# Kernel tuning notes

Measured on AMD Instinct MI355X. Metric: run time of the kernel, lower is better.

## Reference

```python
import jax, jax.numpy as jnp
import numpy as np

MAX_LEN = 1024
DIM = 1024
NUM_HEADS = 16
DIM_HEAD = 64
BATCH = 8


def _pos_emb(max_len, dim):
    pos_seq = jnp.arange(max_len - 1, -1, -1.0, dtype=jnp.float32)
    inv_freq = 1.0 / (10000.0 ** (jnp.arange(0, dim, 2.0, dtype=jnp.float32) / dim))
    sinusoid = jnp.einsum('i,j->ij', pos_seq, inv_freq)
    return jnp.concatenate([jnp.sin(sinusoid), jnp.cos(sinusoid)], axis=-1)  # [S, dim]


def _rel_shift(x):
    # x: [B, H, I, J] -> Transformer-XL relative shift
    b, h, i, j = x.shape
    x = jnp.pad(x, ((0, 0), (0, 0), (0, 0), (1, 0)))
    x = x.reshape(b, h, j + 1, i)[:, :, 1:, :]
    return x.reshape(b, h, i, j)


def setup_inputs() -> dict:
    key = jax.random.key(0)
    k1, k2, k3, k4 = jax.random.split(key, 4)
    inputs = jax.random.normal(k1, (BATCH, MAX_LEN, DIM), dtype=jnp.float32)
    mask = jnp.ones((BATCH, MAX_LEN), dtype=bool)
    Wqkv = jax.random.normal(k2, (DIM, 3 * NUM_HEADS * DIM_HEAD), dtype=jnp.float32) * 0.02
    Wr = jax.random.normal(k3, (DIM, NUM_HEADS * DIM_HEAD), dtype=jnp.float32) * 0.02
    Wo = jax.random.normal(k4, (NUM_HEADS * DIM_HEAD, DIM), dtype=jnp.float32) * 0.02
    return {"inputs": inputs, "mask": mask, "Wqkv": Wqkv, "Wr": Wr, "Wo": Wo}


def reference(inputs, mask, Wqkv, Wr, Wo):
    B, S, dim = inputs.shape
    H, Dh = NUM_HEADS, DIM_HEAD
    scale = 1.0 / (Dh ** 0.5)

    qkv = jnp.einsum('bsd,de->bse', inputs, Wqkv)  # [B,S,3*H*Dh]
    q, k, v = jnp.split(qkv, 3, axis=-1)
    q = q.reshape(B, S, H, Dh)
    k = k.reshape(B, S, H, Dh)
    v = v.reshape(B, S, H, Dh)

    pos = _pos_emb(S, dim)                          # [S, dim]
    r = jnp.einsum('sd,de->se', pos, Wr).reshape(S, H, Dh)  # [S,H,Dh]

    AC = jnp.einsum('bihd,bjhd->bhij', q, k)        # content score
    BD = jnp.einsum('bihd,jhd->bhij', q, r)         # position score
    BD = _rel_shift(BD)
    score = (AC + BD) * scale

    att_mask = mask[:, None, None, :].astype(score.dtype)
    score = score * att_mask - 1e30 * (1.0 - att_mask)

    prob = jax.nn.softmax(score, axis=-1)
    attn_vec = jnp.einsum('bhij,bjhd->bihd', prob, v).reshape(B, S, H * Dh)
    out = jnp.einsum('bse,ed->bsd', attn_vec, Wo)
    return out + inputs
```

## Files before the change

### kernel.cpp

```cpp
#include <hip/hip_runtime.h>

#define SQL 1024
#define NHD 16
#define DHD 64
#define NB  8

typedef unsigned char u8;
typedef unsigned short u16;
typedef short s16x8 __attribute__((ext_vector_type(8)));
typedef __bf16 b16x8 __attribute__((ext_vector_type(8)));
typedef float f32x4 __attribute__((ext_vector_type(4)));
typedef u16 u16x4 __attribute__((ext_vector_type(4)));
typedef u16 u16x8 __attribute__((ext_vector_type(8)));
typedef unsigned int u32x4 __attribute__((ext_vector_type(4)));

static __device__ __forceinline__ u16 f2b(float f) {
  __bf16 h = (__bf16)f;
  return __builtin_bit_cast(u16, h);
}
static __device__ __forceinline__ float b2f(u16 v) {
  return __uint_as_float(((unsigned)v) << 16);
}

#if __has_builtin(__builtin_amdgcn_cvt_pk_fp8_f32)
static __device__ __forceinline__ u8 f2fp8(float f) {
  return (u8)(__builtin_amdgcn_cvt_pk_fp8_f32(f, f, 0, false) & 0xff);
}
#else
static __device__ __forceinline__ u8 f2fp8(float f) {
  f = fminf(fmaxf(f, -448.f), 448.f);
  unsigned s = (__float_as_uint(f) >> 31) << 7;
  float a = fabsf(f);
  if (a < 0.0009765625f) return (u8)s;
  int e; float m = frexpf(a, &e);
  if (e - 1 < -6) {
    int q = (int)(a * 512.f + 0.5f);
    return (u8)(s | q);
  }
  int q = (int)(m * 16.f + 0.5f);
  if (q == 16) { q = 8; ++e; }
  int ef = e - 1 + 7;
  if (ef > 15) { ef = 15; q = 14; }
  return (u8)(s | (ef << 3) | (q - 8));
}
#endif

#if __has_builtin(__builtin_amdgcn_cvt_f32_fp8)
static __device__ __forceinline__ f32x4 fp8dec4(unsigned w) {
  f32x4 r;
  r[0] = __builtin_amdgcn_cvt_f32_fp8(w, 0);
  r[1] = __builtin_amdgcn_cvt_f32_fp8(w, 1);
  r[2] = __builtin_amdgcn_cvt_f32_fp8(w, 2);
  r[3] = __builtin_amdgcn_cvt_f32_fp8(w, 3);
  return r;
}
#else
static __device__ __forceinline__ float fp8dec1(unsigned b) {
  unsigned s = (b >> 7) & 1, e = (b >> 3) & 15, m = b & 7;
  float v = (e == 0) ? (float)m * 0.001953125f
                     : (float)(8 + m) * exp2f((float)((int)e - 10));
  return s ? -v : v;
}
static __device__ __forceinline__ f32x4 fp8dec4(unsigned w) {
  f32x4 r;
  r[0] = fp8dec1(w & 0xff);
  r[1] = fp8dec1((w >> 8) & 0xff);
  r[2] = fp8dec1((w >> 16) & 0xff);
  r[3] = fp8dec1((w >> 24) & 0xff);
  return r;
}
#endif

template <typename V>
static __device__ __forceinline__ auto mfma_sel(V a, V b, f32x4 c, int)
    -> decltype(__builtin_amdgcn_mfma_f32_16x16x32_bf16(a, b, c, 0, 0, 0)) {
  return __builtin_amdgcn_mfma_f32_16x16x32_bf16(a, b, c, 0, 0, 0);
}
template <typename V>
static __device__ __forceinline__ f32x4 mfma_sel(V a, V b, f32x4 c, long) {
  return __builtin_amdgcn_mfma_f32_16x16x32_bf16(
      __builtin_bit_cast(b16x8, a), __builtin_bit_cast(b16x8, b), c, 0, 0, 0);
}
static __device__ __forceinline__ f32x4 MFMA(s16x8 a, s16x8 b, f32x4 c) {
  return mfma_sel(a, b, c, 0);
}

static __device__ __forceinline__ void gload16(const u16* g, u16* l) {
  __builtin_amdgcn_global_load_lds(
      (const __attribute__((address_space(1))) unsigned int*)g,
      (__attribute__((address_space(3))) unsigned int*)l, 16, 0, 0);
}

__global__ __launch_bounds__(256) void cvt_kernel(const float* __restrict__ src,
                                                  u16* __restrict__ dst, int n4) {
  int idx = blockIdx.x * 256 + threadIdx.x;
  if (idx < n4) {
    f32x4 v = reinterpret_cast<const f32x4*>(src)[idx];
    u16x4 o;
    o[0] = f2b(v[0]); o[1] = f2b(v[1]); o[2] = f2b(v[2]); o[3] = f2b(v[3]);
    reinterpret_cast<u16x4*>(dst)[idx] = o;
  }
}

__global__ __launch_bounds__(256) void transpose_cvt(const float* __restrict__ src,
                                                     u16* __restrict__ dst,
                                                     int R, int C) {
  __shared__ float tile[32][33];
  int bx = blockIdx.x * 32;
  int by = blockIdx.y * 32;
  int tx = threadIdx.x & 31, ty = threadIdx.x >> 5;
  #pragma unroll
  for (int r = ty; r < 32; r += 8)
    tile[r][tx] = src[(size_t)(by + r) * C + bx + tx];
  __syncthreads();
  #pragma unroll
  for (int r = ty; r < 32; r += 8)
    dst[(size_t)(bx + r) * R + by + tx] = f2b(tile[tx][r]);
}

__global__ __launch_bounds__(256) void pos_kernel(u16* __restrict__ posb) {
  int idx = blockIdx.x * 256 + threadIdx.x;
  int s = idx >> 10, j = idx & 1023;
  int t = (j < 512) ? j : j - 512;
  float freq = __expf(-(float)(2 * t) * (logf(10000.f) / 1024.f));
  float ang = (float)(1023 - s) * freq;
  posb[idx] = f2b((j < 512) ? sinf(ang) : cosf(ang));
}

__global__ __launch_bounds__(256) void vt_kernel(const u16* __restrict__ qkv,
                                                 u16* __restrict__ vT) {
  int bh = blockIdx.x;
  int b = bh >> 4, h = bh & 15;
  int j0 = blockIdx.y * 64;
  __shared__ __align__(16) u16 tile[64][72];
  int tid = threadIdx.x;
  for (int idx = tid; idx < 512; idx += 256) {
    int j = idx >> 3, c = (idx & 7) * 8;
    *reinterpret_cast<u32x4*>(&tile[j][c]) = *reinterpret_cast<const u32x4*>(
        &qkv[(size_t)(b * SQL + j0 + j) * 3072 + 2048 + h * 64 + c]);
  }
  __syncthreads();
  for (int idx = tid; idx < 512; idx += 256) {
    int d = idx >> 3, c = (idx & 7) * 8;
    u16x8 pk;
    #pragma unroll
    for (int e = 0; e < 8; ++e) pk[e] = tile[c + e][d];
    *reinterpret_cast<u16x8*>(
        &vT[(size_t)bh * DHD * SQL + (size_t)d * SQL + j0 + c]) = pk;
  }
}

template <int OUT>
__global__ __launch_bounds__(256) void gemm97(
    const u16* __restrict__ A, const u16* __restrict__ Bt, void* __restrict__ Cv,
    const float* __restrict__ resid, int K, int lda, int ldb, int ldc,
    int bandH) {
  __shared__ __align__(16) u16 at[128 * 64];
  __shared__ __align__(16) u16 bt[128 * 64];

  int bid = blockIdx.x;
  int xcd = bid & 7, loc = bid >> 3;
  int m0 = (xcd * bandH + (loc % bandH)) * 128;
  int n0 = (loc / bandH) * 128;

  const int tid = threadIdx.x, lane = tid & 63, w = tid >> 6;
  const int wm = (w & 1) * 64, wn = (w >> 1) * 64;
  const int fr = lane & 15, kg = lane >> 4;
  const int lrow = lane >> 3, lcol = (lane & 7) * 8;

  f32x4 acc[4][4] = {};

  for (int k0 = 0; k0 < K; k0 += 64) {
    __syncthreads();
    #pragma unroll
    for (int ci = 0; ci < 4; ++ci) {
      int ch = w * 4 + ci;
      gload16(&A[(size_t)(m0 + ch * 8 + lrow) * lda + k0 + lcol], &at[ch * 512]);
      gload16(&Bt[(size_t)(n0 + ch * 8 + lrow) * ldb + k0 + lcol], &bt[ch * 512]);
    }
    __syncthreads();

    #pragma unroll
    for (int ks = 0; ks < 2; ++ks) {
      s16x8 af[4], bf[4];
      #pragma unroll
      for (int i = 0; i < 4; ++i) {
        af[i] = *(const s16x8*)&at[(wm + i * 16 + fr) * 64 + ks * 32 + kg * 8];
        bf[i] = *(const s16x8*)&bt[(wn + i * 16 + fr) * 64 + ks * 32 + kg * 8];
      }
      #pragma unroll
      for (int mi = 0; mi < 4; ++mi)
        #pragma unroll
        for (int ni = 0; ni < 4; ++ni)
          acc[mi][ni] = MFMA(af[mi], bf[ni], acc[mi][ni]);
    }
  }

  #pragma unroll
  for (int mi = 0; mi < 4; ++mi)
    #pragma unroll
    for (int ni = 0; ni < 4; ++ni)
      #pragma unroll
      for (int rr = 0; rr < 4; ++rr) {
        int rrow = m0 + wm + mi * 16 + kg * 4 + rr;
        int ccol = n0 + wn + ni * 16 + fr;
        size_t ci = (size_t)rrow * ldc + ccol;
        float v = acc[mi][ni][rr];
        if constexpr (OUT == 1) ((u16*)Cv)[ci] = f2b(v);
        else ((float*)Cv)[ci] = v + resid[ci];
      }
}

#define TLD 72
#define SC2 0.180336880f
#define THRU 64.0f

__global__ __launch_bounds__(256, 4) void fused_attn_bd(
    const u16* __restrict__ qkv, const u16* __restrict__ rb,
    u8* __restrict__ cbbd, const u8* __restrict__ cbat,
    const u16* __restrict__ vT, u16* __restrict__ att,
    int zbd, int zat, int nat, int CH) {
  __shared__ __align__(16) u16 smem[13824];
  const int bid = blockIdx.x;
  const int tid = threadIdx.x, lane = tid & 63, w = tid >> 6;
  const int fr = lane & 15, kg = lane >> 4;

  if (bid >= nat) {
    u16* at = smem;
    u16* bt = smem + 5120;
    int loc = bid - nat;
    int zloc = loc >> 6;
    int m0 = (loc & 7) * 128;
    int n0 = ((loc >> 3) & 7) * 128;
    int zg = zbd + zloc;
    int bb = zg >> 4, hh = zg & 15;
    const u16* A = qkv + (size_t)bb * SQL * 3072 + (size_t)hh * 64;
    const u16* Bt = rb + (size_t)hh * 64;
    u8* bd = cbbd + (size_t)zloc * SQL * SQL;

    const int wm = (w >> 1) * 64;
    const int wn = (w & 1) * 64;
    const int kb = kg * 8;

    f32x4 acc[4][4] = {};
    for (int k0 = 0; k0 < 64; k0 += 32) {
      __syncthreads();
      for (int idx = tid; idx < 512; idx += 256) {
        int r = idx >> 2, c = (idx & 3) << 3;
        *(u32x4*)&at[r * 40 + c] =
            *(const u32x4*)&A[(size_t)(m0 + r) * 3072 + k0 + c];
        *(u32x4*)&bt[r * 40 + c] =
            *(const u32x4*)&Bt[(size_t)(n0 + r) * 1024 + k0 + c];
      }
      __syncthreads();

      s16x8 af[4], bfr[4];
      #pragma unroll
      for (int mi = 0; mi < 4; ++mi)
        af[mi] = *(const s16x8*)&at[(wm + mi * 16 + fr) * 40 + kb];
      #pragma unroll
      for (int ni = 0; ni < 4; ++ni)
        bfr[ni] = *(const s16x8*)&bt[(wn + ni * 16 + fr) * 40 + kb];
      #pragma unroll
      for (int mi = 0; mi < 4; ++mi)
        #pragma unroll
        for (int ni = 0; ni < 4; ++ni)
          acc[mi][ni] = MFMA(af[mi], bfr[ni], acc[mi][ni]);
    }

    const int orow = kg << 2;
    const int ocol = fr;
    #pragma unroll
    for (int mi = 0; mi < 4; ++mi)
      #pragma unroll
      for (int ni = 0; ni < 4; ++ni)
        #pragma unroll
        for (int rr = 0; rr < 4; ++rr) {
          int rrow = m0 + wm + mi * 16 + orow + rr;
          int ccol = n0 + wn + ni * 16 + ocol;
          u8 bv = f2fp8(acc[mi][ni][rr]);
          int j1 = rrow + ccol - (SQL - 1);
          if (j1 >= 0) bd[(size_t)rrow * SQL + j1] = bv;
          int j2 = rrow + ccol + 1;
          if (rrow >= 1 && j2 < SQL) bd[(size_t)(rrow - 1) * SQL + j2] = bv;
        }
    if (n0 == 0 && tid < 128) {
      int i = m0 + tid;
      if (i + 1 < SQL) bd[(size_t)i * SQL + i + 1] = 0;
    }
    return;
  }

  u16* kl = smem;
  u16* vl = smem + 4608;
  u16* pl = smem + 9216;

  int per = CH * 2;
  int swz = (bid & 7) * per + (bid >> 3);
  int z = swz >> 4, qt = swz & 15;
  int bh = zat + z;
  int b = bh >> 4, h = bh & 15;
  int i0 = qt * 64;

  const int kb8 = kg * 8;
  const int srow = tid >> 3, sc8 = (tid & 7) * 8;
  const int myrow = w * 16 + fr;

  s16x8 aq[2];
  {
    const u16* qp = &qkv[(size_t)(b * SQL + i0 + myrow) * 3072 + h * 64 + kb8];
    aq[0] = *(const s16x8*)qp;
    aq[1] = *(const s16x8*)(qp + 32);
  }

  const u16* kbase = &qkv[(size_t)(b * SQL) * 3072 + 1024 + h * 64];
  const u16* vbase = &vT[(size_t)bh * 64 * 1024];
  const u8* bdrow = &cbat[(size_t)z * SQL * SQL + (size_t)(i0 + myrow) * SQL + kg * 4];

  u32x4 kA0, kA1, vA0, vA1;
  u32x4 kB0, kB1, vB0, vB1;
  unsigned dA0, dA1, dA2, dA3;
  unsigned dB0, dB1, dB2, dB3;

  auto ISSUE_KV = [&](u32x4& K0, u32x4& K1, u32x4& V0, u32x4& V1, int t) {
    int j0 = t * 64;
    K0 = *(const u32x4*)&kbase[(size_t)(j0 + srow) * 3072 + sc8];
    K1 = *(const u32x4*)&kbase[(size_t)(j0 + srow + 32) * 3072 + sc8];
    V0 = *(const u32x4*)&vbase[(size_t)srow * 1024 + j0 + sc8];
    V1 = *(const u32x4*)&vbase[(size_t)(srow + 32) * 1024 + j0 + sc8];
  };
  auto ISSUE_BD = [&](unsigned& D0, unsigned& D1, unsigned& D2, unsigned& D3,
                      int t) {
    const u8* p = bdrow + t * 64;
    D0 = *(const unsigned*)(p);
    D1 = *(const unsigned*)(p + 16);
    D2 = *(const unsigned*)(p + 32);
    D3 = *(const unsigned*)(p + 48);
  };
  auto COMMIT = [&](u32x4 K0, u32x4 K1, u32x4 V0, u32x4 V1) {
    *(u32x4*)&kl[srow * TLD + sc8] = K0;
    *(u32x4*)&kl[(srow + 32) * TLD + sc8] = K1;
    *(u32x4*)&vl[srow * TLD + sc8] = V0;
    *(u32x4*)&vl[(srow + 32) * TLD + sc8] = V1;
  };

  f32x4 acco[4] = {};
  float mreg = -1e30f, lreg = 0.f;

  auto BODY = [&](int j0, unsigned d0, unsigned d1, unsigned d2, unsigned d3) {
    f32x4 st[4] = {};
    #pragma unroll
    for (int nf = 0; nf < 4; ++nf)
      #pragma unroll
      for (int ks = 0; ks < 2; ++ks)
        st[nf] = MFMA(*(const s16x8*)&kl[(nf * 16 + fr) * TLD + ks * 32 + kb8],
                      aq[ks], st[nf]);

    f32x4 bdv[4] = {fp8dec4(d0), fp8dec4(d1), fp8dec4(d2), fp8dec4(d3)};
    float s0[4][4];
    float rmax = -1e30f;
    #pragma unroll
    for (int nf = 0; nf < 4; ++nf) {
      #pragma unroll
      for (int rr = 0; rr < 4; ++rr) {
        s0[nf][rr] = st[nf][rr] + bdv[nf][rr];
        rmax = fmaxf(rmax, s0[nf][rr]);
      }
    }
    rmax = fmaxf(rmax, __shfl_xor(rmax, 16));
    rmax = fmaxf(rmax, __shfl_xor(rmax, 32));
    if (rmax > mreg + THRU) {
      float sf = exp2f((mreg - rmax) * SC2);
      mreg = rmax;
      lreg *= sf;
      #pragma unroll
      for (int mf = 0; mf < 4; ++mf) acco[mf] *= sf;
    }
    const float C = -mreg * SC2;
    float ps = 0.f;
    #pragma unroll
    for (int nf = 0; nf < 4; ++nf) {
      u16x4 pp;
      #pragma unroll
      for (int rr = 0; rr < 4; ++rr) {
        float p = exp2f(__builtin_fmaf(s0[nf][rr], SC2, C));
        ps += p;
        pp[rr] = f2b(p);
      }
      *(u16x4*)&pl[myrow * TLD + nf * 16 + kg * 4] = pp;
    }
    ps += __shfl_xor(ps, 16);
    ps += __shfl_xor(ps, 32);
    lreg += ps;

    s16x8 ap0 = *(const s16x8*)&pl[myrow * TLD + kb8];
    s16x8 ap1 = *(const s16x8*)&pl[myrow * TLD + 32 + kb8];
    #pragma unroll
    for (int mf = 0; mf < 4; ++mf) {
      acco[mf] = MFMA(*(const s16x8*)&vl[(mf * 16 + fr) * TLD + kb8], ap0,
                      acco[mf]);
      acco[mf] = MFMA(*(const s16x8*)&vl[(mf * 16 + fr) * TLD + 32 + kb8], ap1,
                      acco[mf]);
    }
  };

  ISSUE_KV(kA0, kA1, vA0, vA1, 0);
  ISSUE_BD(dA0, dA1, dA2, dA3, 0);
  for (int tt = 0; tt < 16; tt += 2) {
    __syncthreads();
    COMMIT(kA0, kA1, vA0, vA1);
    __syncthreads();
    ISSUE_KV(kB0, kB1, vB0, vB1, tt + 1);
    ISSUE_BD(dB0, dB1, dB2, dB3, tt + 1);
    BODY(tt * 64, dA0, dA1, dA2, dA3);

    __syncthreads();
    COMMIT(kB0, kB1, vB0, vB1);
    __syncthreads();
    if (tt < 14) {
      ISSUE_KV(kA0, kA1, vA0, vA1, tt + 2);
      ISSUE_BD(dA0, dA1, dA2, dA3, tt + 2);
    }
    BODY((tt + 1) * 64, dB0, dB1, dB2, dB3);
  }

  {
    float inv = 1.0f / lreg;
    size_t base = (size_t)(b * SQL + i0 + myrow) * 1024 + h * 64;
    #pragma unroll
    for (int mf = 0; mf < 4; ++mf) {
      u16x4 o;
      #pragma unroll
      for (int rr = 0; rr < 4; ++rr) o[rr] = f2b(acco[mf][rr] * inv);
      *(u16x4*)&att[base + mf * 16 + kg * 4] = o;
    }
  }
}

extern "C" void kernel_launch(void* const* d_in, const int* in_sizes, int n_in,
                              void* d_out, int out_size, void* d_ws, size_t ws_size,
                              hipStream_t stream) {
  const float* inputs = (const float*)d_in[0];
  const float* Wqkv = (const float*)d_in[2];
  const float* Wr = (const float*)d_in[3];
  const float* Wo = (const float*)d_in[4];
  float* out = (float*)d_out;

  char* ws = (char*)d_ws;
  size_t off = 0;
  auto alloc = [&](size_t bytes) -> char* {
    char* p = ws + off;
    off = (off + bytes + 255) & ~(size_t)255;
    return p;
  };
  u16* qkvb = (u16*)alloc(8192ULL * 3072 * 2);
  u16* vT   = (u16*)alloc(128ULL * 64 * 1024 * 2);
  u16* att  = (u16*)alloc(8192ULL * 1024 * 2);
  u16* rb   = (u16*)alloc(1024ULL * 1024 * 2);
  u16* WoT  = (u16*)alloc(1024ULL * 1024 * 2);

  size_t remain = (ws_size > off) ? (ws_size - off) : 0;
  char* tbase = ws + off;
  u16* Xb    = (u16*)tbase;
  u16* WqkvT = (u16*)(tbase + 16777216);
  u16* WrT   = (u16*)(tbase + 16777216 + 6291456);
  u16* posb  = (u16*)(tbase + 16777216 + 6291456 + 2097152);

  int CH = 8;
  const int cands[4] = {64, 32, 16, 8};
  for (int t = 0; t < 4; ++t) {
    if ((size_t)cands[t] * SQL * SQL * 2 + 1024 <= remain) { CH = cands[t]; break; }
  }
  u8* cbufA = (u8*)tbase;
  u8* cbufB = cbufA + (size_t)CH * SQL * SQL;

  cvt_kernel<<<dim3(8192), dim3(256), 0, stream>>>(inputs, Xb, 8192 * 1024 / 4);
  transpose_cvt<<<dim3(96, 32), dim3(256), 0, stream>>>(Wqkv, WqkvT, 1024, 3072);
  transpose_cvt<<<dim3(32, 32), dim3(256), 0, stream>>>(Wr, WrT, 1024, 1024);
  transpose_cvt<<<dim3(32, 32), dim3(256), 0, stream>>>(Wo, WoT, 1024, 1024);
  pos_kernel<<<dim3(4096), dim3(256), 0, stream>>>(posb);

  gemm97<1><<<dim3(64), dim3(256), 0, stream>>>(
      posb, WrT, rb, nullptr, 1024, 1024, 1024, 1024, 1);
  gemm97<1><<<dim3(1536), dim3(256), 0, stream>>>(
      Xb, WqkvT, qkvb, nullptr, 1024, 1024, 1024, 3072, 8);
  vt_kernel<<<dim3(128, 16), dim3(256), 0, stream>>>(qkvb, vT);

  int nch = 128 / CH;
  for (int r = 0; r <= nch; ++r) {
    int nbd = (r < nch) ? 64 * CH : 0;
    int nat = (r >= 1) ? CH * 16 : 0;
    u8* cbbd = (r & 1) ? cbufB : cbufA;
    u8* cbat = (r & 1) ? cbufA : cbufB;
    fused_attn_bd<<<dim3(nat + nbd), dim3(256), 0, stream>>>(
        qkvb, rb, cbbd, cbat, vT, att, r * CH, (r - 1) * CH, nat, CH);
  }

  gemm97<2><<<dim3(512), dim3(256), 0, stream>>>(
      att, WoT, out, inputs, 1024, 1024, 1024, 1024, 8);
}
```

Before: 341.5 us.

## Store raw BD rows in flat skewed buffer and apply rel-shift at read time

The BD producer blocks now compute Q·R^T per 64-row query tile, streaming R tiles through LDS. They write contiguous rows of packed fp8 (four values per store) into a flat buffer with a 1028-byte row stride, replacing the scattered per-byte writes that applied the relative shift. The attention consumer recovers the shifted values by reading two unaligned word pairs and funnel-shifting them, with a per-element fallback on the diagonal tile. This is meant to cut write traffic and scattered-store cost in the producer. It adds shift and alignment logic and extra loads in the consumer's inner loop.

```diff
diff --git a/kernel.cpp b/kernel.cpp
--- a/kernel.cpp
+++ b/kernel.cpp
@@ -4,9 +4,11 @@
 #define NHD 16
 #define DHD 64
 #define NB  8
+#define HB  1053700ULL
 
 typedef unsigned char u8;
 typedef unsigned short u16;
+typedef unsigned long long u64;
 typedef short s16x8 __attribute__((ext_vector_type(8)));
 typedef __bf16 b16x8 __attribute__((ext_vector_type(8)));
 typedef float f32x4 __attribute__((ext_vector_type(4)));
@@ -23,8 +25,9 @@
 }
 
 #if __has_builtin(__builtin_amdgcn_cvt_pk_fp8_f32)
-static __device__ __forceinline__ u8 f2fp8(float f) {
-  return (u8)(__builtin_amdgcn_cvt_pk_fp8_f32(f, f, 0, false) & 0xff);
+static __device__ __forceinline__ unsigned pack4_fp8(f32x4 v) {
+  unsigned t0 = __builtin_amdgcn_cvt_pk_fp8_f32(v[0], v[1], 0, false);
+  return __builtin_amdgcn_cvt_pk_fp8_f32(v[2], v[3], t0, true);
 }
 #else
 static __device__ __forceinline__ u8 f2fp8(float f) {
@@ -33,15 +36,16 @@
   float a = fabsf(f);
   if (a < 0.0009765625f) return (u8)s;
   int e; float m = frexpf(a, &e);
-  if (e - 1 < -6) {
-    int q = (int)(a * 512.f + 0.5f);
-    return (u8)(s | q);
-  }
+  if (e - 1 < -6) { int q = (int)(a * 512.f + 0.5f); return (u8)(s | q); }
   int q = (int)(m * 16.f + 0.5f);
   if (q == 16) { q = 8; ++e; }
   int ef = e - 1 + 7;
   if (ef > 15) { ef = 15; q = 14; }
   return (u8)(s | (ef << 3) | (q - 8));
+}
+static __device__ __forceinline__ unsigned pack4_fp8(f32x4 v) {
+  return (unsigned)f2fp8(v[0]) | ((unsigned)f2fp8(v[1]) << 8) |
+         ((unsigned)f2fp8(v[2]) << 16) | ((unsigned)f2fp8(v[3]) << 24);
 }
 #endif
 
@@ -53,6 +57,9 @@
   r[2] = __builtin_amdgcn_cvt_f32_fp8(w, 2);
   r[3] = __builtin_amdgcn_cvt_f32_fp8(w, 3);
   return r;
+}
+static __device__ __forceinline__ float fp8dec1(unsigned b) {
+  return __builtin_amdgcn_cvt_f32_fp8(b, 0);
 }
 #else
 static __device__ __forceinline__ float fp8dec1(unsigned b) {
@@ -224,69 +231,62 @@
   const int bid = blockIdx.x;
   const int tid = threadIdx.x, lane = tid & 63, w = tid >> 6;
   const int fr = lane & 15, kg = lane >> 4;
+  const int kb8 = kg * 8;
+  const int srow = tid >> 3, sc8 = (tid & 7) * 8;
+  const int myrow = w * 16 + fr;
 
   if (bid >= nat) {
-    u16* at = smem;
-    u16* bt = smem + 5120;
+    u16* rl = smem;
     int loc = bid - nat;
-    int zloc = loc >> 6;
-    int m0 = (loc & 7) * 128;
-    int n0 = ((loc >> 3) & 7) * 128;
-    int zg = zbd + zloc;
-    int bb = zg >> 4, hh = zg & 15;
-    const u16* A = qkv + (size_t)bb * SQL * 3072 + (size_t)hh * 64;
-    const u16* Bt = rb + (size_t)hh * 64;
-    u8* bd = cbbd + (size_t)zloc * SQL * SQL;
-
-    const int wm = (w >> 1) * 64;
-    const int wn = (w & 1) * 64;
-    const int kb = kg * 8;
-
-    f32x4 acc[4][4] = {};
-    for (int k0 = 0; k0 < 64; k0 += 32) {
+    int z = loc >> 4, qt = loc & 15;
+    int bh = zbd + z;
+    int b = bh >> 4, h = bh & 15;
+    int i0 = qt * 64;
+
+    s16x8 aq[2];
+    {
+      const u16* qp = &qkv[(size_t)(b * SQL + i0 + myrow) * 3072 + h * 64 + kb8];
+      aq[0] = *(const s16x8*)qp;
+      aq[1] = *(const s16x8*)(qp + 32);
+    }
+    const u16* rbase = rb + h * 64;
+    u8* frp = cbbd + (size_t)z * HB + (size_t)(i0 + myrow) * 1028;
+
+    u32x4 rA0, rA1, rB0, rB1;
+    auto ISSUE_R = [&](u32x4& R0, u32x4& R1, int t) {
+      R0 = *(const u32x4*)&rbase[(size_t)(t * 64 + srow) * 1024 + sc8];
+      R1 = *(const u32x4*)&rbase[(size_t)(t * 64 + srow + 32) * 1024 + sc8];
+    };
+    auto COMMIT_R = [&](u32x4 R0, u32x4 R1) {
+      *(u32x4*)&rl[srow * TLD + sc8] = R0;
+      *(u32x4*)&rl[(srow + 32) * TLD + sc8] = R1;
+    };
+    auto CBODY = [&](int mt) {
+      f32x4 ct[4] = {};
+      #pragma unroll
+      for (int nf = 0; nf < 4; ++nf)
+        #pragma unroll
+        for (int ks = 0; ks < 2; ++ks)
+          ct[nf] = MFMA(*(const s16x8*)&rl[(nf * 16 + fr) * TLD + ks * 32 + kb8],
+                        aq[ks], ct[nf]);
+      u8* dst = frp + mt * 64 + kg * 4;
+      #pragma unroll
+      for (int nf = 0; nf < 4; ++nf)
+        *(unsigned*)(dst + nf * 16) = pack4_fp8(ct[nf]);
+    };
+
+    ISSUE_R(rA0, rA1, 0);
+    for (int tt = 0; tt < 16; tt += 2) {
       __syncthreads();
-      for (int idx = tid; idx < 512; idx += 256) {
-        int r = idx >> 2, c = (idx & 3) << 3;
-        *(u32x4*)&at[r * 40 + c] =
-            *(const u32x4*)&A[(size_t)(m0 + r) * 3072 + k0 + c];
-        *(u32x4*)&bt[r * 40 + c] =
-            *(const u32x4*)&Bt[(size_t)(n0 + r) * 1024 + k0 + c];
-      }
+      COMMIT_R(rA0, rA1);
       __syncthreads();
-
-      s16x8 af[4], bfr[4];
-      #pragma unroll
-      for (int mi = 0; mi < 4; ++mi)
-        af[mi] = *(const s16x8*)&at[(wm + mi * 16 + fr) * 40 + kb];
-      #pragma unroll
-      for (int ni = 0; ni < 4; ++ni)
-        bfr[ni] = *(const s16x8*)&bt[(wn + ni * 16 + fr) * 40 + kb];
-      #pragma unroll
-      for (int mi = 0; mi < 4; ++mi)
-        #pragma unroll
-        for (int ni = 0; ni < 4; ++ni)
-          acc[mi][ni] = MFMA(af[mi], bfr[ni], acc[mi][ni]);
-    }
-
-    const int orow = kg << 2;
-    const int ocol = fr;
-    #pragma unroll
-    for (int mi = 0; mi < 4; ++mi)
-      #pragma unroll
-      for (int ni = 0; ni < 4; ++ni)
-        #pragma unroll
-        for (int rr = 0; rr < 4; ++rr) {
-          int rrow = m0 + wm + mi * 16 + orow + rr;
-          int ccol = n0 + wn + ni * 16 + ocol;
-          u8 bv = f2fp8(acc[mi][ni][rr]);
-          int j1 = rrow + ccol - (SQL - 1);
-          if (j1 >= 0) bd[(size_t)rrow * SQL + j1] = bv;
-          int j2 = rrow + ccol + 1;
-          if (rrow >= 1 && j2 < SQL) bd[(size_t)(rrow - 1) * SQL + j2] = bv;
-        }
-    if (n0 == 0 && tid < 128) {
-      int i = m0 + tid;
-      if (i + 1 < SQL) bd[(size_t)i * SQL + i + 1] = 0;
+      ISSUE_R(rB0, rB1, tt + 1);
+      CBODY(tt);
+      __syncthreads();
+      COMMIT_R(rB0, rB1);
+      __syncthreads();
+      if (tt < 14) ISSUE_R(rA0, rA1, tt + 2);
+      CBODY(tt + 1);
     }
     return;
   }
@@ -301,26 +301,26 @@
   int bh = zat + z;
   int b = bh >> 4, h = bh & 15;
   int i0 = qt * 64;
-
-  const int kb8 = kg * 8;
-  const int srow = tid >> 3, sc8 = (tid & 7) * 8;
-  const int myrow = w * 16 + fr;
+  const int ig = i0 + myrow;
 
   s16x8 aq[2];
   {
-    const u16* qp = &qkv[(size_t)(b * SQL + i0 + myrow) * 3072 + h * 64 + kb8];
+    const u16* qp = &qkv[(size_t)(b * SQL + ig) * 3072 + h * 64 + kb8];
     aq[0] = *(const s16x8*)qp;
     aq[1] = *(const s16x8*)(qp + 32);
   }
 
   const u16* kbase = &qkv[(size_t)(b * SQL) * 3072 + 1024 + h * 64];
   const u16* vbase = &vT[(size_t)bh * 64 * 1024];
-  const u8* bdrow = &cbat[(size_t)z * SQL * SQL + (size_t)(i0 + myrow) * SQL + kg * 4];
+  const u8* cbz = cbat + (size_t)z * HB;
+  const size_t Bbase = (size_t)ig * 1027 + 1023 + kg * 4;
+  const unsigned sh1 = (unsigned)(Bbase & 3) * 8;
+  const unsigned sh2 = (unsigned)((Bbase + 3) & 3) * 8;
 
   u32x4 kA0, kA1, vA0, vA1;
   u32x4 kB0, kB1, vB0, vB1;
-  unsigned dA0, dA1, dA2, dA3;
-  unsigned dB0, dB1, dB2, dB3;
+  unsigned a0, a1, a2, a3, a4, a5, a6, a7;
+  unsigned c0, c1, c2, c3, c4, c5, c6, c7;
 
   auto ISSUE_KV = [&](u32x4& K0, u32x4& K1, u32x4& V0, u32x4& V1, int t) {
     int j0 = t * 64;
@@ -329,13 +329,15 @@
     V0 = *(const u32x4*)&vbase[(size_t)srow * 1024 + j0 + sc8];
     V1 = *(const u32x4*)&vbase[(size_t)(srow + 32) * 1024 + j0 + sc8];
   };
-  auto ISSUE_BD = [&](unsigned& D0, unsigned& D1, unsigned& D2, unsigned& D3,
+  auto ISSUE_BD = [&](unsigned& W0, unsigned& W1, unsigned& W2, unsigned& W3,
+                      unsigned& W4, unsigned& W5, unsigned& W6, unsigned& W7,
                       int t) {
-    const u8* p = bdrow + t * 64;
-    D0 = *(const unsigned*)(p);
-    D1 = *(const unsigned*)(p + 16);
-    D2 = *(const unsigned*)(p + 32);
-    D3 = *(const unsigned*)(p + 48);
+    size_t A0 = (Bbase + (size_t)(t * 64) + ((t > qt) ? 3 : 0)) & ~(size_t)3;
+    const u8* p = cbz + A0;
+    W0 = *(const unsigned*)(p);      W1 = *(const unsigned*)(p + 4);
+    W2 = *(const unsigned*)(p + 16); W3 = *(const unsigned*)(p + 20);
+    W4 = *(const unsigned*)(p + 32); W5 = *(const unsigned*)(p + 36);
+    W6 = *(const unsigned*)(p + 48); W7 = *(const unsigned*)(p + 52);
   };
   auto COMMIT = [&](u32x4 K0, u32x4 K1, u32x4 V0, u32x4 V1) {
     *(u32x4*)&kl[srow * TLD + sc8] = K0;
@@ -347,7 +349,8 @@
   f32x4 acco[4] = {};
   float mreg = -1e30f, lreg = 0.f;
 
-  auto BODY = [&](int j0, unsigned d0, unsigned d1, unsigned d2, unsigned d3) {
+  auto BODY = [&](int t, unsigned W0, unsigned W1, unsigned W2, unsigned W3,
+                  unsigned W4, unsigned W5, unsigned W6, unsigned W7) {
     f32x4 st[4] = {};
     #pragma unroll
     for (int nf = 0; nf < 4; ++nf)
@@ -356,7 +359,30 @@
         st[nf] = MFMA(*(const s16x8*)&kl[(nf * 16 + fr) * TLD + ks * 32 + kb8],
                       aq[ks], st[nf]);
 
-    f32x4 bdv[4] = {fp8dec4(d0), fp8dec4(d1), fp8dec4(d2), fp8dec4(d3)};
+    f32x4 bdv[4];
+    if (t == qt) {
+      #pragma unroll
+      for (int nf = 0; nf < 4; ++nf)
+        #pragma unroll
+        for (int rr = 0; rr < 4; ++rr) {
+          int joff = nf * 16 + kg * 4 + rr;
+          float v;
+          if (joff == myrow + 1) v = 0.f;
+          else {
+            size_t P = (size_t)ig * 1027 + (size_t)(qt * 64 + joff) +
+                       ((joff <= myrow) ? 1023 : 1026);
+            v = fp8dec1((unsigned)cbz[P]);
+          }
+          bdv[nf][rr] = v;
+        }
+    } else {
+      unsigned sh = (t > qt) ? sh2 : sh1;
+      bdv[0] = fp8dec4((unsigned)((((u64)W1 << 32) | W0) >> sh));
+      bdv[1] = fp8dec4((unsigned)((((u64)W3 << 32) | W2) >> sh));
+      bdv[2] = fp8dec4((unsigned)((((u64)W5 << 32) | W4) >> sh));
+      bdv[3] = fp8dec4((unsigned)((((u64)W7 << 32) | W6) >> sh));
+    }
+
     float s0[4][4];
     float rmax = -1e30f;
     #pragma unroll
@@ -405,28 +431,28 @@
   };
 
   ISSUE_KV(kA0, kA1, vA0, vA1, 0);
-  ISSUE_BD(dA0, dA1, dA2, dA3, 0);
+  ISSUE_BD(a0, a1, a2, a3, a4, a5, a6, a7, 0);
   for (int tt = 0; tt < 16; tt += 2) {
     __syncthreads();
     COMMIT(kA0, kA1, vA0, vA1);
     __syncthreads();
     ISSUE_KV(kB0, kB1, vB0, vB1, tt + 1);
-    ISSUE_BD(dB0, dB1, dB2, dB3, tt + 1);
-    BODY(tt * 64, dA0, dA1, dA2, dA3);
+    ISSUE_BD(c0, c1, c2, c3, c4, c5, c6, c7, tt + 1);
+    BODY(tt, a0, a1, a2, a3, a4, a5, a6, a7);
 
     __syncthreads();
     COMMIT(kB0, kB1, vB0, vB1);
     __syncthreads();
     if (tt < 14) {
       ISSUE_KV(kA0, kA1, vA0, vA1, tt + 2);
-      ISSUE_BD(dA0, dA1, dA2, dA3, tt + 2);
-    }
-    BODY((tt + 1) * 64, dB0, dB1, dB2, dB3);
+      ISSUE_BD(a0, a1, a2, a3, a4, a5, a6, a7, tt + 2);
+    }
+    BODY(tt + 1, c0, c1, c2, c3, c4, c5, c6, c7);
   }
 
   {
     float inv = 1.0f / lreg;
-    size_t base = (size_t)(b * SQL + i0 + myrow) * 1024 + h * 64;
+    size_t base = (size_t)(b * SQL + ig) * 1024 + h * 64;
     #pragma unroll
     for (int mf = 0; mf < 4; ++mf) {
       u16x4 o;
@@ -469,10 +495,10 @@
   int CH = 8;
   const int cands[4] = {64, 32, 16, 8};
   for (int t = 0; t < 4; ++t) {
-    if ((size_t)cands[t] * SQL * SQL * 2 + 1024 <= remain) { CH = cands[t]; break; }
+    if ((size_t)cands[t] * HB * 2 + 1024 <= remain) { CH = cands[t]; break; }
   }
   u8* cbufA = (u8*)tbase;
-  u8* cbufB = cbufA + (size_t)CH * SQL * SQL;
+  u8* cbufB = cbufA + (size_t)CH * HB;
 
   cvt_kernel<<<dim3(8192), dim3(256), 0, stream>>>(inputs, Xb, 8192 * 1024 / 4);
   transpose_cvt<<<dim3(96, 32), dim3(256), 0, stream>>>(Wqkv, WqkvT, 1024, 3072);
@@ -488,7 +514,7 @@
 
   int nch = 128 / CH;
   for (int r = 0; r <= nch; ++r) {
-    int nbd = (r < nch) ? 64 * CH : 0;
+    int nbd = (r < nch) ? CH * 16 : 0;
     int nat = (r >= 1) ? CH * 16 : 0;
     u8* cbbd = (r & 1) ? cbufB : cbufA;
     u8* cbat = (r & 1) ? cbufA : cbufB;
```

Result: slower. 437.5 us (+28.1%).
